# Kernel tuning notes

Hardware: AMD Instinct MI355X
Metric: run time of the kernel (lower is better)

## Reference

```python
import jax, jax.numpy as jnp
import numpy as np

B, C, H, W = 4, 512, 56, 56
G, K = 16, 3
P = K * K
GC = C // G
DWK = 3
PAD = 1
OFFSET_SCALE = 1.0


def setup_inputs():
    key = jax.random.key(0)
    ks = jax.random.split(key, 10)

    def w(i, shape, sc=0.02):
        return jax.random.normal(ks[i], shape, jnp.float32) * sc

    return {
        "x": jax.random.normal(ks[0], (B, C, H, W), jnp.float32),
        "w_in": w(1, (C, C)), "b_in": jnp.zeros((C,), jnp.float32),
        "w_dw": w(2, (DWK, DWK, 1, C)), "b_dw": jnp.zeros((C,), jnp.float32),
        "ln_g": jnp.ones((C,), jnp.float32), "ln_b": jnp.zeros((C,), jnp.float32),
        "w_off": w(3, (C, G * P * 2)), "b_off": jnp.zeros((G * P * 2,), jnp.float32),
        "w_mask": w(4, (C, G * P)), "b_mask": jnp.zeros((G * P,), jnp.float32),
        "w_out": w(5, (C, C)), "b_out": jnp.zeros((C,), jnp.float32),
        "bn_g": jnp.ones((C,), jnp.float32), "bn_b": jnp.zeros((C,), jnp.float32),
        "bn_m": w(6, (C,), 0.1), "bn_v": jnp.abs(w(7, (C,), 0.1)) + 1.0,
    }


def _dcnv3_core(xp, offset, mask):
    """xp: [B,H,W,C]; offset: [B,H,W,G*P*2]; mask (softmaxed over P): [B,H,W,G,P]."""
    xpad = jnp.pad(xp, ((0, 0), (PAD, PAD), (PAD, PAD), (0, 0)))
    Hin, Win = H + 2 * PAD, W + 2 * PAD
    # normalized reference points (output-location centers in padded input coords)
    ref_x = (jnp.arange(W, dtype=jnp.float32) + 0.5 + (K - 1) // 2) / Win
    ref_y = (jnp.arange(H, dtype=jnp.float32) + 0.5 + (K - 1) // 2) / Hin
    # dilation grid, kx-major / ky-minor flattening (matches InternImage core)
    k = jnp.arange(K, dtype=jnp.float32) - (K - 1) // 2
    gx = jnp.repeat(k, K) / Win  # [P]
    gy = jnp.tile(k, K) / Hin    # [P]
    off = offset.reshape(B, H, W, G, P, 2)
    lx = ref_x[None, None, :, None, None] + gx * OFFSET_SCALE + off[..., 0] * OFFSET_SCALE / Win
    ly = ref_y[None, :, None, None, None] + gy * OFFSET_SCALE + off[..., 1] * OFFSET_SCALE / Hin
    # grid_sample semantics, align_corners=False, zero padding
    px = lx * Win - 0.5
    py = ly * Hin - 0.5
    x0f = jnp.floor(px)
    y0f = jnp.floor(py)
    tx = px - x0f
    ty = py - y0f
    x0 = x0f.astype(jnp.int32)
    y0 = y0f.astype(jnp.int32)
    flat = xpad.reshape(B, Hin * Win * G, GC)
    gidx = jnp.arange(G)[None, None, :, None]

    def corner(fb, yi, xi):
        valid = (yi >= 0) & (yi < Hin) & (xi >= 0) & (xi < Win)
        idx = (jnp.clip(yi, 0, Hin - 1) * Win + jnp.clip(xi, 0, Win - 1)) * G + gidx
        return jnp.take(fb, idx, axis=0) * valid[..., None]  # [H,W,G,P,GC]

    def sample_one(fb, y0b, x0b, tyb, txb):
        w00 = ((1 - tyb) * (1 - txb))[..., None]
        w01 = ((1 - tyb) * txb)[..., None]
        w10 = (tyb * (1 - txb))[..., None]
        w11 = (tyb * txb)[..., None]
        return (corner(fb, y0b, x0b) * w00 + corner(fb, y0b, x0b + 1) * w01
                + corner(fb, y0b + 1, x0b) * w10 + corner(fb, y0b + 1, x0b + 1) * w11)

    samp = jax.vmap(sample_one)(flat, y0, x0, ty, tx)  # [B,H,W,G,P,GC]
    return jnp.einsum('bhwgpc,bhwgp->bhwgc', samp, mask).reshape(B, H, W, C)


def reference(x, w_in, b_in, w_dw, b_dw, ln_g, ln_b, w_off, b_off, w_mask, b_mask, w_out, b_out, bn_g, bn_b, bn_m, bn_v):
    xh = jnp.transpose(x, (0, 2, 3, 1))  # NCHW -> NHWC
    xp = xh @ w_in + b_in                # input_proj
    # offset/mask branch: depthwise conv + LayerNorm(channels) + GELU
    x1 = jax.lax.conv_general_dilated(xh, w_dw, (1, 1), 'SAME', feature_group_count=C,
                                      dimension_numbers=('NHWC', 'HWIO', 'NHWC')) + b_dw
    mu = x1.mean(-1, keepdims=True)
    var = x1.var(-1, keepdims=True)
    x1 = (x1 - mu) / jnp.sqrt(var + 1e-6) * ln_g + ln_b
    x1 = jax.nn.gelu(x1, approximate=False)
    offset = x1 @ w_off + b_off
    mask = jax.nn.softmax((x1 @ w_mask + b_mask).reshape(B, H, W, G, P), axis=-1)
    y = _dcnv3_core(xp, offset, mask)
    y = y @ w_out + b_out                # output_proj
    y = jnp.transpose(y, (0, 3, 1, 2))   # NHWC -> NCHW
    # BatchNorm2d (inference: running stats) + SiLU
    y = (y - bn_m[:, None, None]) / jnp.sqrt(bn_v[:, None, None] + 1e-5) * bn_g[:, None, None] + bn_b[:, None, None]
    return jax.nn.silu(y)
```

## Files before the change

kernel.cpp:

```cpp
#include <hip/hip_runtime.h>
#include <cmath>

constexpr int B_ = 4, C_ = 512, H_ = 56, W_ = 56;
constexpr int HW_ = H_ * W_;
constexpr int NPIX = B_ * HW_;
constexpr int G_ = 16, P_ = 9;
constexpr int NMSK = G_ * P_;
constexpr int GEMM_BLOCKS = 1568;
constexpr int TRANS_BLOCKS = (HW_ / 32) * (C_ / 32) * B_;
constexpr int PREP_BLOCKS = 16 * 16 * 3;

typedef __attribute__((ext_vector_type(8))) short short8;
typedef __attribute__((ext_vector_type(4))) float f32x4;

__device__ __forceinline__ float b2f(ushort u) {
    union { unsigned int i; float f; } v; v.i = (unsigned int)u << 16; return v.f;
}
__device__ __forceinline__ ushort f2b(float f) {
    unsigned int x = __float_as_uint(f);
    unsigned int r = (x + 0x7fffu + ((x >> 16) & 1u)) >> 16;
    return (ushort)r;
}
__device__ __forceinline__ void gload16(const ushort* g, ushort* l) {
    __builtin_amdgcn_global_load_lds(
        (const __attribute__((address_space(1))) unsigned int*)g,
        (__attribute__((address_space(3))) unsigned int*)l, 16, 0, 0);
}

union GemmSMem {
    struct { ushort As[64 * 64]; ushort Bs[64 * 64]; } s;
    float eb[64 * 67];
};

__global__ __launch_bounds__(256) void pre_kernel(
    const float* __restrict__ x, ushort* __restrict__ xh,
    const float* __restrict__ w_in, const float* __restrict__ w_off,
    const float* __restrict__ w_mask, const float* __restrict__ w_out,
    const float* __restrict__ b_off, const float* __restrict__ b_mask,
    ushort* __restrict__ wtA, ushort* __restrict__ wtOM, ushort* __restrict__ wtO,
    float* __restrict__ bOM)
{
    __shared__ float tile[32][33];
    int bid = blockIdx.x;
    int tx = threadIdx.x, ty = threadIdx.y;
    if (bid < TRANS_BLOCKS) {
        int bx = bid % 98;
        int rem = bid / 98;
        int by = rem % 16;
        int bz = rem / 16;
        int hw0 = bx * 32, c0 = by * 32;
        const float* ib = x + (size_t)bz * C_ * HW_;
        #pragma unroll
        for (int i = ty; i < 32; i += 8)
            tile[i][tx] = ib[(size_t)(c0 + i) * HW_ + hw0 + tx];
        __syncthreads();
        ushort* ob = xh + (size_t)bz * HW_ * C_;
        #pragma unroll
        for (int i = ty; i < 32; i += 8)
            ob[(size_t)(hw0 + i) * C_ + c0 + tx] = f2b(tile[tx][i]);
    } else {
        int p = bid - TRANS_BLOCKS;
        int px = p % 16;
        int py = (p / 16) % 16;
        int pz = p / 256;
        int k0 = px * 32;
        int n0 = py * 32;
        for (int i = ty; i < 32; i += 8) {
            int k = k0 + i, n = n0 + tx;
            float v;
            if (pz == 0) v = w_in[k * 512 + n];
            else if (pz == 1) v = w_out[k * 512 + n];
            else v = (n < 288) ? w_off[k * 288 + n]
                               : (n < 432 ? w_mask[k * 144 + (n - 288)] : 0.f);
            tile[i][tx] = v;
        }
        __syncthreads();
        ushort* dst = (pz == 0) ? wtA : (pz == 1 ? wtO : wtOM);
        for (int i = ty; i < 32; i += 8)
            dst[(size_t)(n0 + i) * 512 + k0 + tx] = f2b(tile[tx][i]);
        if (pz == 2 && px == 0 && py == 0) {
            int t = ty * 32 + tx;
            for (int tt = t; tt < 512; tt += 256)
                bOM[tt] = (tt < 288) ? b_off[tt] : (tt < 432 ? b_mask[tt - 288] : 0.f);
        }
    }
}

template <int MODE>
__device__ __forceinline__ void gemm_body(
    ushort* __restrict__ As, ushort* __restrict__ Bs, float* __restrict__ ebf,
    int wgid, const ushort* __restrict__ A, const ushort* __restrict__ Bt,
    const float* __restrict__ bias, void* __restrict__ Cout,
    const float* __restrict__ bng, const float* __restrict__ bnb,
    const float* __restrict__ bnm, const float* __restrict__ bnv)
{
    int tid = threadIdx.x;
    int lane = tid & 63, wid = tid >> 6;
    int row0 = (wgid >> 3) * 64, col0 = (wgid & 7) * 64;
    int wm = wid >> 1, wn = wid & 1;

    f32x4 acc[2][2] = {};

    int lr = lane >> 3;
    int sc = (lane & 7) ^ lr;

    for (int k0 = 0; k0 < 512; k0 += 64) {
        if (k0) __syncthreads();
        #pragma unroll
        for (int i = 0; i < 2; i++) {
            int s = wid * 2 + i;
            gload16(A + (size_t)(row0 + s * 8 + lr) * 512 + k0 + sc * 8, &As[s * 512]);
            gload16(Bt + (size_t)(col0 + s * 8 + lr) * 512 + k0 + sc * 8, &Bs[s * 512]);
        }
        __syncthreads();
        #pragma unroll
        for (int ks = 0; ks < 2; ks++) {
            short8 af[2], bf[2];
            #pragma unroll
            for (int mi = 0; mi < 2; mi++) {
                int r = wm * 32 + mi * 16 + (lane & 15);
                int c = ((lane >> 4) + ks * 4) ^ (r & 7);
                af[mi] = *(const short8*)((const char*)As + r * 128 + c * 16);
            }
            #pragma unroll
            for (int ni = 0; ni < 2; ni++) {
                int r = wn * 32 + ni * 16 + (lane & 15);
                int c = ((lane >> 4) + ks * 4) ^ (r & 7);
                bf[ni] = *(const short8*)((const char*)Bs + r * 128 + c * 16);
            }
            #pragma unroll
            for (int mi = 0; mi < 2; mi++)
                #pragma unroll
                for (int ni = 0; ni < 2; ni++)
                    acc[mi][ni] = __builtin_amdgcn_mfma_f32_16x16x32_bf16(
                        af[mi], bf[ni], acc[mi][ni], 0, 0, 0);
        }
    }

    if constexpr (MODE == 2) {
        __syncthreads();
        #pragma unroll
        for (int ni = 0; ni < 2; ni++) {
            int cl = wn * 32 + ni * 16 + (lane & 15);
            int col = col0 + cl;
            float bv = bias[col];
            float inv = rsqrtf(bnv[col] + 1e-5f);
            float bsc = bng[col] * inv;
            float bsh = bnb[col] - bnm[col] * bsc;
            int rl = (lane >> 4) * 4;
            #pragma unroll
            for (int mi = 0; mi < 2; mi++)
                #pragma unroll
                for (int r = 0; r < 4; r++) {
                    float val = acc[mi][ni][r] + bv;
                    float t2 = val * bsc + bsh;
                    float s = t2 / (1.f + expf(-t2));
                    ebf[cl * 67 + wm * 32 + mi * 16 + rl + r] = s;
                }
        }
        __syncthreads();
        int bb = row0 / HW_;
        int hw0 = row0 - bb * HW_;
        float* ob = (float*)Cout + (size_t)bb * C_ * HW_ + hw0 + lane;
        #pragma unroll
        for (int it = 0; it < 16; it++) {
            int chan = it * 4 + wid;
            ob[(size_t)(col0 + chan) * HW_] = ebf[chan * 67 + lane];
        }
    } else {
        #pragma unroll
        for (int ni = 0; ni < 2; ni++) {
            int col = col0 + wn * 32 + ni * 16 + (lane & 15);
            float bv = bias[col];
            #pragma unroll
            for (int mi = 0; mi < 2; mi++) {
                int rowb = row0 + wm * 32 + mi * 16 + (lane >> 4) * 4;
                #pragma unroll
                for (int r = 0; r < 4; r++) {
                    float val = acc[mi][ni][r] + bv;
                    if constexpr (MODE == 0)
                        ((float*)Cout)[(size_t)(rowb + r) * 512 + col] = val;
                    else
                        ((ushort*)Cout)[(size_t)(rowb + r) * 512 + col] = f2b(val);
                }
            }
        }
    }
}

template <int MODE>
__global__ __launch_bounds__(256) void mfma_gemm_kernel(
    const ushort* __restrict__ A, const ushort* __restrict__ Bt,
    const float* __restrict__ bias, void* __restrict__ Cout,
    const float* __restrict__ bng, const float* __restrict__ bnb,
    const float* __restrict__ bnm, const float* __restrict__ bnv)
{
    __shared__ GemmSMem sm;
    int bid = blockIdx.x;
    int wgid = (bid & 7) * (GEMM_BLOCKS / 8) + (bid >> 3);
    gemm_body<MODE>(sm.s.As, sm.s.Bs, sm.eb, wgid,
                    A, Bt, bias, Cout, bng, bnb, bnm, bnv);
}

__device__ __forceinline__ void dwln_body(
    int bid, const ushort* __restrict__ xh, const float* __restrict__ wdw,
    const float* __restrict__ bdw, const float* __restrict__ lng,
    const float* __restrict__ lnb, ushort* __restrict__ x1)
{
    int tid = threadIdx.x;
    int wid = tid >> 6, lane = tid & 63;
    int j = (bid & 7) * (NPIX / 32) + (bid >> 3);
    int n = j * 4 + wid;
    int b = n / HW_, hw = n % HW_;
    int h = hw / W_, w = hw % W_;
    int c0 = lane * 8;
    const ushort* base = xh + (size_t)b * HW_ * C_ + c0;

    uint4 nb[9];
    #pragma unroll
    for (int ky = 0; ky < 3; ky++)
        #pragma unroll
        for (int kx = 0; kx < 3; kx++) {
            int hh = h + ky - 1, ww = w + kx - 1;
            bool ok = (hh >= 0) & (hh < H_) & (ww >= 0) & (ww < W_);
            nb[ky * 3 + kx] = ok ? *(const uint4*)(base + ((size_t)hh * W_ + ww) * C_)
                                 : make_uint4(0u, 0u, 0u, 0u);
        }

    float acc[8];
    {
        float4 b0 = *(const float4*)&bdw[c0];
        float4 b1 = *(const float4*)&bdw[c0 + 4];
        acc[0] = b0.x; acc[1] = b0.y; acc[2] = b0.z; acc[3] = b0.w;
        acc[4] = b1.x; acc[5] = b1.y; acc[6] = b1.z; acc[7] = b1.w;
    }
    #pragma unroll
    for (int p = 0; p < 9; p++) {
        float4 w0 = *(const float4*)&wdw[p * C_ + c0];
        float4 w1 = *(const float4*)&wdw[p * C_ + c0 + 4];
        float wv[8] = {w0.x, w0.y, w0.z, w0.w, w1.x, w1.y, w1.z, w1.w};
        unsigned int u[4] = {nb[p].x, nb[p].y, nb[p].z, nb[p].w};
        #pragma unroll
        for (int q = 0; q < 4; q++) {
            float lo = __uint_as_float(u[q] << 16);
            float hi = __uint_as_float(u[q] & 0xffff0000u);
            acc[2 * q]     += wv[2 * q]     * lo;
            acc[2 * q + 1] += wv[2 * q + 1] * hi;
        }
    }

    float s1 = 0.f, s2 = 0.f;
    #pragma unroll
    for (int q = 0; q < 8; q++) { s1 += acc[q]; s2 += acc[q] * acc[q]; }
    #pragma unroll
    for (int o = 32; o > 0; o >>= 1) {
        s1 += __shfl_xor(s1, o);
        s2 += __shfl_xor(s2, o);
    }
    float mean = s1 * (1.f / 512.f);
    float var = s2 * (1.f / 512.f) - mean * mean;
    float inv = rsqrtf(var + 1e-6f);

    float4 g0 = *(const float4*)&lng[c0];
    float4 g1 = *(const float4*)&lng[c0 + 4];
    float4 e0 = *(const float4*)&lnb[c0];
    float4 e1 = *(const float4*)&lnb[c0 + 4];
    float gv[8] = {g0.x, g0.y, g0.z, g0.w, g1.x, g1.y, g1.z, g1.w};
    float ev[8] = {e0.x, e0.y, e0.z, e0.w, e1.x, e1.y, e1.z, e1.w};
    unsigned int outw[4];
    #pragma unroll
    for (int q = 0; q < 4; q++) {
        float t0 = (acc[2 * q]     - mean) * inv * gv[2 * q]     + ev[2 * q];
        float t1 = (acc[2 * q + 1] - mean) * inv * gv[2 * q + 1] + ev[2 * q + 1];
        float ge0 = 0.5f * t0 * (1.f + erff(t0 * 0.70710678118654752f));
        float ge1 = 0.5f * t1 * (1.f + erff(t1 * 0.70710678118654752f));
        outw[q] = (unsigned int)f2b(ge0) | ((unsigned int)f2b(ge1) << 16);
    }
    *(uint4*)&x1[(size_t)n * C_ + c0] = make_uint4(outw[0], outw[1], outw[2], outw[3]);
}

__global__ __launch_bounds__(256) void g1_dwln_kernel(
    const ushort* __restrict__ xh, const ushort* __restrict__ wtA,
    const float* __restrict__ b_in, ushort* __restrict__ xpb,
    const float* __restrict__ wdw, const float* __restrict__ bdw,
    const float* __restrict__ lng, const float* __restrict__ lnb,
    ushort* __restrict__ x1)
{
    __shared__ GemmSMem sm;
    int bid = blockIdx.x;
    if (bid < GEMM_BLOCKS) {
        int wgid = (bid & 7) * (GEMM_BLOCKS / 8) + (bid >> 3);
        gemm_body<1>(sm.s.As, sm.s.Bs, sm.eb, wgid,
                     xh, wtA, b_in, xpb, nullptr, nullptr, nullptr, nullptr);
    } else {
        dwln_body(bid - GEMM_BLOCKS, xh, wdw, bdw, lng, lnb, x1);
    }
}

__global__ __launch_bounds__(256) void dcn_sample_kernel(
    const ushort* __restrict__ xp, const ushort* __restrict__ om,
    ushort* __restrict__ y1)
{
    __shared__ float slog[NMSK];
    __shared__ float sw4[NMSK][4];
    __shared__ int   sa4[NMSK][4];
    int bid = blockIdx.x;
    int n = (bid & 7) * (NPIX / 8) + (bid >> 3);
    int b = n / HW_, hw = n % HW_;
    int h = hw / W_, w = hw % W_;
    int tid = threadIdx.x;
    const ushort* omp = om + (size_t)n * 512;

    if (tid < NMSK) slog[tid] = b2f(omp[288 + tid]);
    __syncthreads();
    if (tid < G_) {
        float mx = -1e30f;
        #pragma unroll
        for (int p = 0; p < P_; p++) mx = fmaxf(mx, slog[tid * P_ + p]);
        float e[P_], s = 0.f;
        #pragma unroll
        for (int p = 0; p < P_; p++) { e[p] = expf(slog[tid * P_ + p] - mx); s += e[p]; }
        float invs = 1.f / s;
        #pragma unroll
        for (int p = 0; p < P_; p++) slog[tid * P_ + p] = e[p] * invs;
    }
    __syncthreads();
    if (tid < NMSK) {
        int g = tid / 9, p = tid - g * 9;
        float ox = b2f(omp[g * 18 + p * 2 + 0]);
        float oy = b2f(omp[g * 18 + p * 2 + 1]);
        float px = (float)(w + (p / 3)) + ox;
        float py = (float)(h + (p % 3)) + oy;
        float x0f = floorf(px), y0f = floorf(py);
        float tx = px - x0f, ty = py - y0f;
        int x0 = (int)x0f, y0 = (int)y0f;
        float m = slog[tid];
        float ww[4] = { (1.f - ty) * (1.f - tx) * m, (1.f - ty) * tx * m,
                        ty * (1.f - tx) * m,         ty * tx * m };
        #pragma unroll
        for (int i = 0; i < 4; i++) {
            int yy = y0 + (i >> 1), xx = x0 + (i & 1);
            bool valid = (yy >= 1 && yy <= H_ && xx >= 1 && xx <= W_);
            sa4[tid][i] = valid ? ((yy - 1) * W_ + (xx - 1)) * C_ : 0;
            sw4[tid][i] = valid ? ww[i] : 0.f;
        }
    }
    __syncthreads();

    const ushort* xpb = xp + (size_t)b * HW_ * C_;
    int c0 = tid * 2;
    int g = tid >> 4;

    int addr[P_][4];
    #pragma unroll
    for (int p = 0; p < P_; p++)
        #pragma unroll
        for (int i = 0; i < 4; i++)
            addr[p][i] = sa4[g * 9 + p][i] + c0;

    unsigned int v[P_][4];
    #pragma unroll
    for (int p = 0; p < P_; p++)
        #pragma unroll
        for (int i = 0; i < 4; i++)
            v[p][i] = *(const unsigned int*)(xpb + addr[p][i]);

    float ax = 0.f, ay = 0.f;
    #pragma unroll
    for (int p = 0; p < P_; p++)
        #pragma unroll
        for (int i = 0; i < 4; i++) {
            float wgt = sw4[g * 9 + p][i];
            float lo = __uint_as_float(v[p][i] << 16);
            float hi = __uint_as_float(v[p][i] & 0xffff0000u);
            ax += wgt * lo;
            ay += wgt * hi;
        }

    ushort2 o; o.x = f2b(ax); o.y = f2b(ay);
    *(ushort2*)&y1[(size_t)n * 512 + c0] = o;
}

extern "C" void kernel_launch(void* const* d_in, const int* in_sizes, int n_in,
                              void* d_out, int out_size, void* d_ws, size_t ws_size,
                              hipStream_t stream)
{
    const float* x      = (const float*)d_in[0];
    const float* w_in   = (const float*)d_in[1];
    const float* b_in   = (const float*)d_in[2];
    const float* w_dw   = (const float*)d_in[3];
    const float* b_dw   = (const float*)d_in[4];
    const float* ln_g   = (const float*)d_in[5];
    const float* ln_b   = (const float*)d_in[6];
    const float* w_off  = (const float*)d_in[7];
    const float* b_off  = (const float*)d_in[8];
    const float* w_mask = (const float*)d_in[9];
    const float* b_mask = (const float*)d_in[10];
    const float* w_out  = (const float*)d_in[11];
    const float* b_out  = (const float*)d_in[12];
    const float* bn_g   = (const float*)d_in[13];
    const float* bn_b   = (const float*)d_in[14];
    const float* bn_m   = (const float*)d_in[15];
    const float* bn_v   = (const float*)d_in[16];
    float* out = (float*)d_out;

    const size_t NC = (size_t)NPIX * C_;
    char* wsp = (char*)d_ws;
    ushort* xh  = (ushort*)wsp;  wsp += NC * 2;
    ushort* x1  = (ushort*)wsp;  wsp += NC * 2;
    ushort* xpb = (ushort*)wsp;  wsp += NC * 2;
    ushort* om  = (ushort*)wsp;  wsp += NC * 2;
    ushort* wtA = (ushort*)wsp;  wsp += 512 * 512 * 2;
    ushort* wtOM= (ushort*)wsp;  wsp += 512 * 512 * 2;
    ushort* wtO = (ushort*)wsp;  wsp += 512 * 512 * 2;
    float*  bOM = (float*)wsp;   wsp += 512 * 4;

    dim3 tb(32, 8);
    pre_kernel<<<TRANS_BLOCKS + PREP_BLOCKS, tb, 0, stream>>>(
        x, xh, w_in, w_off, w_mask, w_out, b_off, b_mask, wtA, wtOM, wtO, bOM);

    g1_dwln_kernel<<<GEMM_BLOCKS + NPIX / 4, 256, 0, stream>>>(
        xh, wtA, b_in, xpb, w_dw, b_dw, ln_g, ln_b, x1);

    mfma_gemm_kernel<1><<<GEMM_BLOCKS, 256, 0, stream>>>(
        x1, wtOM, bOM, om, nullptr, nullptr, nullptr, nullptr);

    dcn_sample_kernel<<<NPIX, 256, 0, stream>>>(xpb, om, x1 );

    mfma_gemm_kernel<2><<<GEMM_BLOCKS, 256, 0, stream>>>(
        x1, wtO, b_out, out, bn_g, bn_b, bn_m, bn_v);
}
```

Baseline: 108.2 us.

## Interleave offset/mask weights per group and compute sampling coords per thread without LDS

The packed offset/mask projection weights and bias are reordered so each group's 18 offsets and 9 mask logits sit in a contiguous 32-column slot. The sampling kernel then has every thread load its group's 32 values with four vector loads, compute the softmax and the bilinear addresses and weights itself, and skip the shared-memory staging and three block barriers. This removes the serialized setup phases where only a few threads worked. In exchange, the softmax and coordinate math is repeated 16 times per group and register pressure rises.

```diff
diff --git a/kernel.cpp b/kernel.cpp
--- a/kernel.cpp
+++ b/kernel.cpp
@@ -5,7 +5,6 @@
 constexpr int HW_ = H_ * W_;
 constexpr int NPIX = B_ * HW_;
 constexpr int G_ = 16, P_ = 9;
-constexpr int NMSK = G_ * P_;
 constexpr int GEMM_BLOCKS = 1568;
 constexpr int TRANS_BLOCKS = (HW_ / 32) * (C_ / 32) * B_;
 constexpr int PREP_BLOCKS = 16 * 16 * 3;
@@ -70,8 +69,11 @@
             float v;
             if (pz == 0) v = w_in[k * 512 + n];
             else if (pz == 1) v = w_out[k * 512 + n];
-            else v = (n < 288) ? w_off[k * 288 + n]
-                               : (n < 432 ? w_mask[k * 144 + (n - 288)] : 0.f);
+            else {
+                int g = n >> 5, r = n & 31;
+                v = (r < 18) ? w_off[k * 288 + g * 18 + r]
+                  : (r < 27) ? w_mask[k * 144 + g * 9 + (r - 18)] : 0.f;
+            }
             tile[i][tx] = v;
         }
         __syncthreads();
@@ -80,8 +82,11 @@
             dst[(size_t)(n0 + i) * 512 + k0 + tx] = f2b(tile[tx][i]);
         if (pz == 2 && px == 0 && py == 0) {
             int t = ty * 32 + tx;
-            for (int tt = t; tt < 512; tt += 256)
-                bOM[tt] = (tt < 288) ? b_off[tt] : (tt < 432 ? b_mask[tt - 288] : 0.f);
+            for (int tt = t; tt < 512; tt += 256) {
+                int g = tt >> 5, r = tt & 31;
+                bOM[tt] = (r < 18) ? b_off[g * 18 + r]
+                        : (r < 27) ? b_mask[g * 9 + (r - 18)] : 0.f;
+            }
         }
     }
 }
@@ -301,80 +306,73 @@
     const ushort* __restrict__ xp, const ushort* __restrict__ om,
     ushort* __restrict__ y1)
 {
-    __shared__ float slog[NMSK];
-    __shared__ float sw4[NMSK][4];
-    __shared__ int   sa4[NMSK][4];
     int bid = blockIdx.x;
     int n = (bid & 7) * (NPIX / 8) + (bid >> 3);
     int b = n / HW_, hw = n % HW_;
     int h = hw / W_, w = hw % W_;
     int tid = threadIdx.x;
-    const ushort* omp = om + (size_t)n * 512;
-
-    if (tid < NMSK) slog[tid] = b2f(omp[288 + tid]);
-    __syncthreads();
-    if (tid < G_) {
-        float mx = -1e30f;
-        #pragma unroll
-        for (int p = 0; p < P_; p++) mx = fmaxf(mx, slog[tid * P_ + p]);
-        float e[P_], s = 0.f;
-        #pragma unroll
-        for (int p = 0; p < P_; p++) { e[p] = expf(slog[tid * P_ + p] - mx); s += e[p]; }
-        float invs = 1.f / s;
-        #pragma unroll
-        for (int p = 0; p < P_; p++) slog[tid * P_ + p] = e[p] * invs;
-    }
-    __syncthreads();
-    if (tid < NMSK) {
-        int g = tid / 9, p = tid - g * 9;
-        float ox = b2f(omp[g * 18 + p * 2 + 0]);
-        float oy = b2f(omp[g * 18 + p * 2 + 1]);
+    int g = tid >> 4;
+    int c0 = tid * 2;
+
+    const ushort* omg = om + (size_t)n * 512 + g * 32;
+    union { uint4 v4[4]; unsigned int d[16]; } u;
+    u.v4[0] = *(const uint4*)(omg);
+    u.v4[1] = *(const uint4*)(omg + 8);
+    u.v4[2] = *(const uint4*)(omg + 16);
+    u.v4[3] = *(const uint4*)(omg + 24);
+    float vals[28];
+    #pragma unroll
+    for (int i = 0; i < 14; i++) {
+        vals[2 * i]     = b2f((ushort)(u.d[i] & 0xffffu));
+        vals[2 * i + 1] = b2f((ushort)(u.d[i] >> 16));
+    }
+
+    float mx = vals[18];
+    #pragma unroll
+    for (int p = 1; p < 9; p++) mx = fmaxf(mx, vals[18 + p]);
+    float e[9], s = 0.f;
+    #pragma unroll
+    for (int p = 0; p < 9; p++) { e[p] = expf(vals[18 + p] - mx); s += e[p]; }
+    float invs = 1.f / s;
+
+    const ushort* xpb = xp + (size_t)b * HW_ * C_;
+    float wgt[9][4];
+    int   adr[9][4];
+    #pragma unroll
+    for (int p = 0; p < 9; p++) {
+        float ox = vals[p * 2], oy = vals[p * 2 + 1];
         float px = (float)(w + (p / 3)) + ox;
         float py = (float)(h + (p % 3)) + oy;
         float x0f = floorf(px), y0f = floorf(py);
         float tx = px - x0f, ty = py - y0f;
         int x0 = (int)x0f, y0 = (int)y0f;
-        float m = slog[tid];
-        float ww[4] = { (1.f - ty) * (1.f - tx) * m, (1.f - ty) * tx * m,
+        float m = e[p] * invs;
+        float wv[4] = { (1.f - ty) * (1.f - tx) * m, (1.f - ty) * tx * m,
                         ty * (1.f - tx) * m,         ty * tx * m };
         #pragma unroll
-        for (int i = 0; i < 4; i++) {
-            int yy = y0 + (i >> 1), xx = x0 + (i & 1);
+        for (int q = 0; q < 4; q++) {
+            int yy = y0 + (q >> 1), xx = x0 + (q & 1);
             bool valid = (yy >= 1 && yy <= H_ && xx >= 1 && xx <= W_);
-            sa4[tid][i] = valid ? ((yy - 1) * W_ + (xx - 1)) * C_ : 0;
-            sw4[tid][i] = valid ? ww[i] : 0.f;
-        }
-    }
-    __syncthreads();
-
-    const ushort* xpb = xp + (size_t)b * HW_ * C_;
-    int c0 = tid * 2;
-    int g = tid >> 4;
-
-    int addr[P_][4];
-    #pragma unroll
-    for (int p = 0; p < P_; p++)
-        #pragma unroll
-        for (int i = 0; i < 4; i++)
-            addr[p][i] = sa4[g * 9 + p][i] + c0;
-
-    unsigned int v[P_][4];
-    #pragma unroll
-    for (int p = 0; p < P_; p++)
-        #pragma unroll
-        for (int i = 0; i < 4; i++)
-            v[p][i] = *(const unsigned int*)(xpb + addr[p][i]);
+            adr[p][q] = valid ? ((yy - 1) * W_ + (xx - 1)) * C_ + c0 : c0;
+            wgt[p][q] = valid ? wv[q] : 0.f;
+        }
+    }
+
+    unsigned int v[9][4];
+    #pragma unroll
+    for (int p = 0; p < 9; p++)
+        #pragma unroll
+        for (int q = 0; q < 4; q++)
+            v[p][q] = *(const unsigned int*)(xpb + adr[p][q]);
 
     float ax = 0.f, ay = 0.f;
     #pragma unroll
-    for (int p = 0; p < P_; p++)
-        #pragma unroll
-        for (int i = 0; i < 4; i++) {
-            float wgt = sw4[g * 9 + p][i];
-            float lo = __uint_as_float(v[p][i] << 16);
-            float hi = __uint_as_float(v[p][i] & 0xffff0000u);
-            ax += wgt * lo;
-            ay += wgt * hi;
+    for (int p = 0; p < 9; p++)
+        #pragma unroll
+        for (int q = 0; q < 4; q++) {
+            float wq = wgt[p][q];
+            ax += wq * __uint_as_float(v[p][q] << 16);
+            ay += wq * __uint_as_float(v[p][q] & 0xffff0000u);
         }
 
     ushort2 o; o.x = f2b(ax); o.y = f2b(ay);
```

Measured after the change: 141.3 us. 30.5% more time.
